# Optimization experiments

Measured on AMD Instinct MI355X. Metric: run time of the kernel, lower is better.

The kernel has to match this reference:

```python
import jax, jax.numpy as jnp
import numpy as np

N_COMPANY = 16384
N_SECTOR = 64
PER_SECTOR = N_COMPANY // N_SECTOR  # 256, companies grouped contiguously by sector
WIN = 32
D_IN = 16
H_GRU = 64
H_INTRA = 64
H_INTER = 64
D_OUT = 4
E_INNER = 524288  # avg degree 32 within sectors


def setup_inputs() -> dict:
    key = jax.random.key(0)
    ks = jax.random.split(key, 20)
    s = 0.05

    daily_data_batch = jax.random.normal(ks[0], (WIN, N_COMPANY, D_IN), jnp.float32)

    rng = np.random.default_rng(0)
    dst = rng.integers(0, N_COMPANY, E_INNER)
    src = (dst // PER_SECTOR) * PER_SECTOR + rng.integers(0, PER_SECTOR, E_INNER)  # same-sector neighbors
    inner_edge = jnp.asarray(np.stack([src, dst]), jnp.int32)

    a, b = np.meshgrid(np.arange(N_SECTOR), np.arange(N_SECTOR), indexing="ij")
    oe = np.stack([a.ravel(), b.ravel()])
    oe = oe[:, oe[0] != oe[1]]  # fully-connected sector graph w/o self loops (GAT adds them)
    outer_edge = jnp.asarray(oe, jnp.int32)

    sector_ids = jnp.asarray(np.arange(N_COMPANY) // PER_SECTOR, jnp.int32)

    inp = {
        "daily_data_batch": daily_data_batch,
        "inner_edge": inner_edge,
        "outer_edge": outer_edge,
        "sector_ids": sector_ids,
        # BatchNorm1d(input_dim*window_size)
        "bn_gamma": jnp.ones((D_IN * WIN,), jnp.float32),
        "bn_beta": jnp.zeros((D_IN * WIN,), jnp.float32),
        # Graph GRU (per-node learnable initial hidden state)
        "gru_Wih": s * jax.random.normal(ks[1], (D_IN, 3 * H_GRU), jnp.float32),
        "gru_Whh": s * jax.random.normal(ks[2], (H_GRU, 3 * H_GRU), jnp.float32),
        "gru_bih": jnp.zeros((3 * H_GRU,), jnp.float32),
        "gru_bhh": jnp.zeros((3 * H_GRU,), jnp.float32),
        "gru_h0": s * jax.random.normal(ks[3], (N_COMPANY, H_GRU), jnp.float32),
        # intra-sector GATConv
        "gat1_W": s * jax.random.normal(ks[4], (H_GRU, H_INTRA), jnp.float32),
        "gat1_asrc": s * jax.random.normal(ks[5], (H_INTRA,), jnp.float32),
        "gat1_adst": s * jax.random.normal(ks[6], (H_INTRA,), jnp.float32),
        "gat1_b": jnp.zeros((H_INTRA,), jnp.float32),
        # inter-sector GATConv
        "gat2_W": s * jax.random.normal(ks[7], (H_INTRA, H_INTER), jnp.float32),
        "gat2_asrc": s * jax.random.normal(ks[8], (H_INTER,), jnp.float32),
        "gat2_adst": s * jax.random.normal(ks[9], (H_INTER,), jnp.float32),
        "gat2_b": jnp.zeros((H_INTER,), jnp.float32),
        # fusion / logit heads
        "fusion_W": s * jax.random.normal(ks[10], (H_GRU + H_INTRA + H_INTER, H_GRU), jnp.float32),
        "fusion_b": jnp.zeros((H_GRU,), jnp.float32),
        "logit_W": s * jax.random.normal(ks[11], (H_GRU, D_OUT), jnp.float32),
        "logit_b": jnp.zeros((D_OUT,), jnp.float32),
    }
    return inp


def _gat(x, edge, W, a_src, a_dst, b):
    """PyG-style single-head GATConv with default add_self_loops=True."""
    N = x.shape[0]
    h = x @ W  # [N, F]
    loops = jnp.arange(N, dtype=edge.dtype)
    src = jnp.concatenate([edge[0], loops])
    dst = jnp.concatenate([edge[1], loops])
    e = jax.nn.leaky_relu(h[src] @ a_src + h[dst] @ a_dst, 0.2)  # [E]
    # segment softmax over incoming edges per dst node
    m = jax.ops.segment_max(e, dst, num_segments=N)
    ex = jnp.exp(e - m[dst])
    denom = jax.ops.segment_sum(ex, dst, num_segments=N)
    alpha = ex / (denom[dst] + 1e-16)
    out = jax.ops.segment_sum(h[src] * alpha[:, None], dst, num_segments=N)
    return out + b


def _forward(daily_data_batch, inner_edge, outer_edge, sector_ids,
             bn_gamma, bn_beta,
             gru_Wih, gru_Whh, gru_bih, gru_bhh, gru_h0,
             gat1_W, gat1_asrc, gat1_adst, gat1_b,
             gat2_W, gat2_asrc, gat2_adst, gat2_b,
             fusion_W, fusion_b, logit_W, logit_b):
    W, N, D = daily_data_batch.shape
    # BatchNorm1d over companies (train-mode batch stats, eps=1e-5)
    xb = jnp.transpose(daily_data_batch, (1, 0, 2)).reshape(N, W * D)
    mu = xb.mean(axis=0)
    var = xb.var(axis=0)
    xb = (xb - mu) * jax.lax.rsqrt(var + 1e-5) * bn_gamma + bn_beta
    x = jnp.transpose(xb.reshape(N, W, D), (1, 0, 2))  # [W, N, D]

    # GRU over the window, per-node hidden state
    def step(h, xt):
        gi = xt @ gru_Wih + gru_bih
        gh = h @ gru_Whh + gru_bhh
        ir, iz, inn = jnp.split(gi, 3, axis=-1)
        hr, hz, hn = jnp.split(gh, 3, axis=-1)
        r = jax.nn.sigmoid(ir + hr)
        z = jax.nn.sigmoid(iz + hz)
        n = jnp.tanh(inn + r * hn)
        return (1.0 - z) * n + z * h, None

    seq_emb, _ = jax.lax.scan(step, gru_h0, x)  # [N, H_GRU]

    intra_emb = _gat(seq_emb, inner_edge, gat1_W, gat1_asrc, gat1_adst, gat1_b)  # [N, H_INTRA]

    # sector_separater + per-sector max pooling == segment_max
    sec_pool = jax.ops.segment_max(intra_emb, sector_ids, num_segments=N_SECTOR)  # [S, H_INTRA]
    sec_emb = _gat(sec_pool, outer_edge, gat2_W, gat2_asrc, gat2_adst, gat2_b)  # [S, H_INTER]
    sec_broad = sec_emb[sector_ids]  # repeat_interleave back to companies

    fusion_vec = jnp.concatenate([seq_emb, sec_broad, intra_emb], axis=-1)
    fusion_vec = jax.nn.relu(fusion_vec @ fusion_W + fusion_b)
    logits = jax.nn.softmax(fusion_vec @ logit_W + logit_b, axis=1)
    logits = jnp.cumsum(logits, axis=1)
    eps = 5e-08
    return jnp.clip(logits, eps, 1.0 - eps)


def reference(daily_data_batch, inner_edge, outer_edge, sector_ids,
              bn_gamma, bn_beta,
              gru_Wih, gru_Whh, gru_bih, gru_bhh, gru_h0,
              gat1_W, gat1_asrc, gat1_adst, gat1_b,
              gat2_W, gat2_asrc, gat2_adst, gat2_b,
              fusion_W, fusion_b, logit_W, logit_b):
    return _forward(daily_data_batch, inner_edge, outer_edge, sector_ids,
                    bn_gamma, bn_beta,
                    gru_Wih, gru_Whh, gru_bih, gru_bhh, gru_h0,
                    gat1_W, gat1_asrc, gat1_adst, gat1_b,
                    gat2_W, gat2_asrc, gat2_adst, gat2_b,
                    fusion_W, fusion_b, logit_W, logit_b)
```

## Files before the change

### kernel.cpp

```cpp
#include <hip/hip_runtime.h>

#define NC 16384
#define WIN 32
#define DI 16
#define EI 524288

typedef unsigned short u16;
typedef unsigned char u8;
typedef unsigned int u32;
typedef __attribute__((ext_vector_type(8))) short bfrag8;
typedef __attribute__((ext_vector_type(4))) float facc4;

__device__ __forceinline__ float bf2f(u16 u) { return __uint_as_float(((u32)u) << 16); }
__device__ __forceinline__ u16 f2bf(float f) {
    u32 u = __float_as_uint(f);
    u += 0x7FFFu + ((u >> 16) & 1u);
    return (u16)(u >> 16);
}
__device__ __forceinline__ float frcp(float x) { return __builtin_amdgcn_rcpf(x); }
__device__ __forceinline__ float ex2(float x) {
#if __has_builtin(__builtin_amdgcn_exp2f)
    return __builtin_amdgcn_exp2f(x);
#else
    return __expf(x * 0.69314718055994531f);
#endif
}
__device__ __forceinline__ u32 pk2bf(float a, float b) {
    u32 r;
    asm("v_cvt_pk_bf16_f32 %0, %1, %2" : "=v"(r) : "v"(a), "v"(b));
    return r;
}
__device__ __forceinline__ float lrelu(float x) { return x >= 0.0f ? x : 0.2f * x; }
__device__ __forceinline__ float loadf(const void* p, size_t i, bool f32) {
    return f32 ? ((const float*)p)[i] : bf2f(((const u16*)p)[i]);
}
__device__ __forceinline__ bool is_f32(const void* gamma) {
    return ((const u32*)gamma)[0] == 0x3F800000u;
}
__device__ __forceinline__ int hswz(int f, int s) { return s ^ (((f >> 3) & 3) << 3); }

#define O_WIMG  1024
#define O_BIMG  10240
#define O_BIH   16384
#define O_BHH   16576
#define O_G1W   16768
#define O_G1AS  20864
#define O_G1AD  20928
#define O_G1B   20992
#define O_G2W   21056
#define O_G2AS  25152
#define O_G2AD  25216
#define O_G2B   25280
#define O_FB    25344
#define O_LW    25408
#define O_LB    25664
#define O_FW16  25668
#define O_BNACC 31812
#define O_SEQ   40960
#define O_H1    1089536
#define O_INTRA 1613824
#define O_SPOOL 2138112
#define O_AS    2170880
#define O_AD    2187264
#define O_M     2203648

__global__ __launch_bounds__(256) void k_convert(const void* __restrict__ daily,
                                                 const int* __restrict__ edges,
                                                 u32* __restrict__ M32,
                                                 const void* __restrict__ gamma,
                                                 const void* __restrict__ wih,
                                                 const void* __restrict__ whh,
                                                 const void* __restrict__ bih,
                                                 const void* __restrict__ bhh,
                                                 const void* __restrict__ g1w,
                                                 const void* __restrict__ g1as,
                                                 const void* __restrict__ g1ad,
                                                 const void* __restrict__ g1b,
                                                 const void* __restrict__ g2w,
                                                 const void* __restrict__ g2as,
                                                 const void* __restrict__ g2ad,
                                                 const void* __restrict__ g2b,
                                                 const void* __restrict__ fw,
                                                 const void* __restrict__ fb,
                                                 const void* __restrict__ lw,
                                                 const void* __restrict__ lb,
                                                 float* __restrict__ ws) {
    __shared__ float rS[256 * 17];
    __shared__ float rQ[256 * 17];
    __shared__ float sOut[2][16][16];
    int bid = blockIdx.x;
    int tid = threadIdx.x;
    int gt = bid * 256 + tid;
    const int GS = 640 * 256;
    bool f32 = is_f32(gamma);
    const float KR = -1.4426950408889634f;
    const float KN = -2.8853900817779268f;

    if (bid >= 128) {
        int g = (bid - 128) * 256 + tid;
        int4 s4 = ((const int4*)edges)[g];
        int4 d4 = ((const int4*)(edges + EI))[g];
        int ss[4] = {s4.x, s4.y, s4.z, s4.w};
        int dd[4] = {d4.x, d4.y, d4.z, d4.w};
#pragma unroll
        for (int i = 0; i < 4; i++) {
            int sl = ss[i] & 255;
            atomicAdd(&M32[dd[i] * 64 + (sl >> 2)], 1u << ((sl & 3) * 8));
        }
        return;
    }

    u16* fw16 = (u16*)(ws + O_FW16);
    for (int i = gt; i < 12288; i += GS)
        fw16[i] = f32 ? f2bf(((const float*)fw)[i]) : ((const u16*)fw)[i];
    for (int i = gt; i < 4096; i += GS) {
        ws[O_G1W + i] = loadf(g1w, i, f32);
        ws[O_G2W + i] = loadf(g2w, i, f32);
    }
    if (gt < 64) {
        ws[O_G1AS + gt] = loadf(g1as, gt, f32);
        ws[O_G1AD + gt] = loadf(g1ad, gt, f32);
        ws[O_G1B + gt] = loadf(g1b, gt, f32);
        ws[O_G2AS + gt] = loadf(g2as, gt, f32);
        ws[O_G2AD + gt] = loadf(g2ad, gt, f32);
        ws[O_G2B + gt] = loadf(g2b, gt, f32);
        ws[O_FB + gt] = loadf(fb, gt, f32);
    }
    if (gt < 256) ws[O_LW + gt] = loadf(lw, gt, f32);
    if (gt < 4) ws[O_LB + gt] = loadf(lb, gt, f32);

    for (int i = gt; i < 9216; i += GS) {
        int trow = i / 36;
        int idx = i % 36;
        int w_ = trow >> 6, lane_ = trow & 63, li_ = lane_ & 15, q_ = lane_ >> 4;
        u16 lo, hi;
        if (idx < 24) {
            int g = idx >> 3, kc = (idx >> 2) & 1, j2 = idx & 3;
            float sc = (g < 2) ? KR : KN;
            int col = g * 64 + w_ * 16 + li_;
            int k = kc * 32 + q_ * 8 + j2 * 2;
            lo = f2bf(sc * loadf(whh, (size_t)k * 192 + col, f32));
            hi = f2bf(sc * loadf(whh, (size_t)(k + 1) * 192 + col, f32));
        } else {
            int idx2 = idx - 24;
            int g = idx2 >> 2, j2 = idx2 & 3;
            float sc = (g < 2) ? KR : KN;
            int col = g * 64 + w_ * 16 + li_;
            int k = q_ * 8 + j2 * 2;
            lo = (k < 16) ? f2bf(sc * loadf(wih, (size_t)k * 192 + col, f32)) : (u16)0;
            hi = (k + 1 < 16) ? f2bf(sc * loadf(wih, (size_t)(k + 1) * 192 + col, f32)) : (u16)0;
        }
        ((u32*)(ws + O_WIMG))[i] = (u32)lo | ((u32)hi << 16);
    }
    for (int i = gt; i < 1024; i += GS) {
        int trow = i >> 2, e = i & 3;
        int w_ = trow >> 6, lane_ = trow & 63, li_ = lane_ & 15;
        int c = w_ * 16 + li_;
        float v;
        if (e == 0) v = KR * (loadf(bih, c, f32) + loadf(bhh, c, f32));
        else if (e == 1) v = KR * (loadf(bih, 64 + c, f32) + loadf(bhh, 64 + c, f32));
        else if (e == 2) v = KN * loadf(bih, 128 + c, f32);
        else v = KN * loadf(bhh, 128 + c, f32);
        ws[O_BIMG + i] = v;
    }

    {
        int w = bid >> 2, ch = bid & 3;
        float s[16], q[16];
#pragma unroll
        for (int i = 0; i < 16; i++) { s[i] = 0.f; q[i] = 0.f; }
        for (int it = 0; it < 16; it++) {
            int c = ch * 4096 + it * 256 + tid;
            size_t base = ((size_t)w * NC + c) * DI;
            float v[16];
            if (f32) {
                const float4* p = (const float4*)((const float*)daily + base);
                float4 a = p[0], b = p[1], cc = p[2], d = p[3];
                v[0] = a.x; v[1] = a.y; v[2] = a.z; v[3] = a.w;
                v[4] = b.x; v[5] = b.y; v[6] = b.z; v[7] = b.w;
                v[8] = cc.x; v[9] = cc.y; v[10] = cc.z; v[11] = cc.w;
                v[12] = d.x; v[13] = d.y; v[14] = d.z; v[15] = d.w;
            } else {
                const uint4* p = (const uint4*)((const u16*)daily + base);
                uint4 a = p[0], b = p[1];
                u32 us[8] = {a.x, a.y, a.z, a.w, b.x, b.y, b.z, b.w};
#pragma unroll
                for (int i = 0; i < 8; i++) {
                    v[2 * i] = __uint_as_float(us[i] << 16);
                    v[2 * i + 1] = __uint_as_float(us[i] & 0xFFFF0000u);
                }
            }
#pragma unroll
            for (int i = 0; i < 16; i++) { s[i] += v[i]; q[i] += v[i] * v[i]; }
        }
#pragma unroll
        for (int i = 0; i < 16; i++) { rS[tid * 17 + i] = s[i]; rQ[tid * 17 + i] = q[i]; }
        __syncthreads();
        int f = tid & 15, g = tid >> 4;
        float ss = 0.f, qq = 0.f;
        for (int t = g * 16; t < g * 16 + 16; t++) { ss += rS[t * 17 + f]; qq += rQ[t * 17 + f]; }
        sOut[0][g][f] = ss;
        sOut[1][g][f] = qq;
        __syncthreads();
        if (tid < 16) {
            float S = 0.f, Q = 0.f;
#pragma unroll
            for (int g2 = 0; g2 < 16; g2++) { S += sOut[0][g2][tid]; Q += sOut[1][g2][tid]; }
            ws[O_BNACC + ch * 512 + w * 16 + tid] = S;
            ws[O_BNACC + 2048 + ch * 512 + w * 16 + tid] = Q;
        }
    }
}

__global__ __launch_bounds__(256) void k_gru(const void* __restrict__ daily,
                                             const void* __restrict__ gamma,
                                             const void* __restrict__ beta,
                                             const void* __restrict__ h0_g,
                                             const float* __restrict__ ws,
                                             float* __restrict__ seq_out,
                                             u16* __restrict__ h1_out,
                                             float* __restrict__ asg,
                                             float* __restrict__ adg) {
    __shared__ __attribute__((aligned(16))) u16 sHd[2][16 * 72];
    __shared__ __attribute__((aligned(16))) u16 sXall[512 * 24];
    __shared__ float sSc[512], sSh[512];
    __shared__ float sRed[2][4][16];
    int tid = threadIdx.x;
    int w = tid >> 6, lane = tid & 63;
    int li = lane & 15, q = lane >> 4;
    int n0 = blockIdx.x * 16;
    int colw = w * 16 + li;
    bool f32 = is_f32(gamma);

    for (int f = tid; f < 512; f += 256) {
        float S = ws[O_BNACC + f] + ws[O_BNACC + 512 + f] + ws[O_BNACC + 1024 + f] + ws[O_BNACC + 1536 + f];
        float Q = ws[O_BNACC + 2048 + f] + ws[O_BNACC + 2560 + f] + ws[O_BNACC + 3072 + f] + ws[O_BNACC + 3584 + f];
        float mu = S * (1.0f / NC);
        float var = Q * (1.0f / NC) - mu * mu;
        float sc = loadf(gamma, f, f32) * rsqrtf(var + 1e-5f);
        sSc[f] = sc;
        sSh[f] = loadf(beta, f, f32) - mu * sc;
    }
    __syncthreads();

    for (int R = tid; R < 512; R += 256) {
        int t = R >> 4, m = R & 15;
        size_t base = ((size_t)t * NC + n0 + m) * DI;
        float xv[16];
        if (f32) {
            const float4* p = (const float4*)((const float*)daily + base);
            float4 a = p[0], b = p[1], c = p[2], d = p[3];
            xv[0] = a.x; xv[1] = a.y; xv[2] = a.z; xv[3] = a.w;
            xv[4] = b.x; xv[5] = b.y; xv[6] = b.z; xv[7] = b.w;
            xv[8] = c.x; xv[9] = c.y; xv[10] = c.z; xv[11] = c.w;
            xv[12] = d.x; xv[13] = d.y; xv[14] = d.z; xv[15] = d.w;
        } else {
            const uint4* p = (const uint4*)((const u16*)daily + base);
            uint4 a = p[0], b = p[1];
            u32 us[8] = {a.x, a.y, a.z, a.w, b.x, b.y, b.z, b.w};
#pragma unroll
            for (int i = 0; i < 8; i++) {
                xv[2 * i] = __uint_as_float(us[i] << 16);
                xv[2 * i + 1] = __uint_as_float(us[i] & 0xFFFF0000u);
            }
        }
        u32 pxu[8];
#pragma unroll
        for (int i = 0; i < 16; i += 2)
            pxu[i >> 1] = pk2bf(xv[i] * sSc[t * 16 + i] + sSh[t * 16 + i],
                                xv[i + 1] * sSc[t * 16 + i + 1] + sSh[t * 16 + i + 1]);
        *(uint4*)&sXall[R * 24] = *(const uint4*)&pxu[0];
        *(uint4*)&sXall[R * 24 + 8] = *(const uint4*)&pxu[4];
    }

    bfrag8 bh[3][2];
    bfrag8 bx[3];
    {
        const bfrag8* wf = (const bfrag8*)((const char*)(ws + O_WIMG) + (size_t)tid * 144);
        int c_ = 0;
#pragma unroll
        for (int g = 0; g < 3; g++)
#pragma unroll
            for (int kc = 0; kc < 2; kc++) bh[g][kc] = wf[c_++];
#pragma unroll
        for (int g = 0; g < 3; g++) bx[g] = wf[c_++];
    }
    float bR, bZ, bNX, bNH;
    {
        float4 b0 = ((const float4*)(ws + O_BIMG))[tid];
        bR = b0.x; bZ = b0.y; bNX = b0.z; bNH = b0.w;
    }

    float hC[4];
#pragma unroll
    for (int r = 0; r < 4; r++)
        hC[r] = loadf(h0_g, (size_t)(n0 + q * 4 + r) * 64 + colw, f32);
    {
        int hr = tid >> 4, hc = (tid & 15) * 4;
        u32 a = pk2bf(loadf(h0_g, (size_t)(n0 + hr) * 64 + hc, f32),
                      loadf(h0_g, (size_t)(n0 + hr) * 64 + hc + 1, f32));
        u32 b = pk2bf(loadf(h0_g, (size_t)(n0 + hr) * 64 + hc + 2, f32),
                      loadf(h0_g, (size_t)(n0 + hr) * 64 + hc + 3, f32));
        uint2 v2; v2.x = a; v2.y = b;
        *(uint2*)&sHd[0][hr * 72 + hc] = v2;
    }
    __syncthreads();

    bfrag8 ax = (bfrag8){0, 0, 0, 0, 0, 0, 0, 0};
    if (q < 2) ax = *(const bfrag8*)&sXall[li * 24 + q * 8];
    for (int t = 0; t < WIN; t++) {
        int p = t & 1;
        bfrag8 ah0 = *(const bfrag8*)&sHd[p][li * 72 + q * 8];
        bfrag8 ah1 = *(const bfrag8*)&sHd[p][li * 72 + 32 + q * 8];
        int tn = (t + 1) & (WIN - 1);
        bfrag8 axn = (bfrag8){0, 0, 0, 0, 0, 0, 0, 0};
        if (q < 2) axn = *(const bfrag8*)&sXall[(tn * 16 + li) * 24 + q * 8];
        facc4 aR = __builtin_amdgcn_mfma_f32_16x16x32_bf16(ax, bx[0], (facc4){bR, bR, bR, bR}, 0, 0, 0);
        facc4 aZ = __builtin_amdgcn_mfma_f32_16x16x32_bf16(ax, bx[1], (facc4){bZ, bZ, bZ, bZ}, 0, 0, 0);
        facc4 aNX = __builtin_amdgcn_mfma_f32_16x16x32_bf16(ax, bx[2], (facc4){bNX, bNX, bNX, bNX}, 0, 0, 0);
        facc4 aNH = __builtin_amdgcn_mfma_f32_16x16x32_bf16(ah0, bh[2][0], (facc4){bNH, bNH, bNH, bNH}, 0, 0, 0);
        aR = __builtin_amdgcn_mfma_f32_16x16x32_bf16(ah0, bh[0][0], aR, 0, 0, 0);
        aZ = __builtin_amdgcn_mfma_f32_16x16x32_bf16(ah0, bh[1][0], aZ, 0, 0, 0);
        aNH = __builtin_amdgcn_mfma_f32_16x16x32_bf16(ah1, bh[2][1], aNH, 0, 0, 0);
        aR = __builtin_amdgcn_mfma_f32_16x16x32_bf16(ah1, bh[0][1], aR, 0, 0, 0);
        aZ = __builtin_amdgcn_mfma_f32_16x16x32_bf16(ah1, bh[1][1], aZ, 0, 0, 0);
#pragma unroll
        for (int r = 0; r < 4; r++) {
            float gr = frcp(1.0f + ex2(aR[r]));
            float gz = frcp(1.0f + ex2(aZ[r]));
            float narg = aNX[r] + gr * aNH[r];
            float gn = 2.0f * frcp(1.0f + ex2(narg)) - 1.0f;
            hC[r] = gn + gz * (hC[r] - gn);
        }
#pragma unroll
        for (int rp = 0; rp < 4; rp += 2) {
            u32 pk = pk2bf(hC[rp], hC[rp + 1]);
            sHd[p ^ 1][(q * 4 + rp) * 72 + colw] = (u16)pk;
            sHd[p ^ 1][(q * 4 + rp + 1) * 72 + colw] = (u16)(pk >> 16);
        }
        __syncthreads();
        ax = axn;
    }

#pragma unroll
    for (int r = 0; r < 4; r++)
        seq_out[(size_t)(n0 + q * 4 + r) * 64 + colw] = hC[r];

    bfrag8 a0 = *(const bfrag8*)&sHd[0][li * 72 + q * 8];
    bfrag8 a1 = *(const bfrag8*)&sHd[0][li * 72 + 32 + q * 8];
    const facc4 zf = {0.f, 0.f, 0.f, 0.f};
    bfrag8 bg0, bg1;
#pragma unroll
    for (int j = 0; j < 8; j++) {
        bg0[j] = (short)f2bf(ws[O_G1W + (q * 8 + j) * 64 + colw]);
        bg1[j] = (short)f2bf(ws[O_G1W + (32 + q * 8 + j) * 64 + colw]);
    }
    facc4 acc = __builtin_amdgcn_mfma_f32_16x16x32_bf16(a0, bg0, zf, 0, 0, 0);
    acc = __builtin_amdgcn_mfma_f32_16x16x32_bf16(a1, bg1, acc, 0, 0, 0);
    float a1s_j = ws[O_G1AS + colw], a1d_j = ws[O_G1AD + colw];
    float pAs[4], pAd[4];
#pragma unroll
    for (int r = 0; r < 4; r++) {
        h1_out[(size_t)(n0 + q * 4 + r) * 64 + colw] = f2bf(acc[r]);
        pAs[r] = acc[r] * a1s_j;
        pAd[r] = acc[r] * a1d_j;
    }
#pragma unroll
    for (int o = 1; o < 16; o <<= 1)
#pragma unroll
        for (int r = 0; r < 4; r++) {
            pAs[r] += __shfl_xor(pAs[r], o);
            pAd[r] += __shfl_xor(pAd[r], o);
        }
    if (li == 0) {
#pragma unroll
        for (int r = 0; r < 4; r++) {
            sRed[0][w][q * 4 + r] = pAs[r];
            sRed[1][w][q * 4 + r] = pAd[r];
        }
    }
    __syncthreads();
    if (tid < 16) {
        asg[n0 + tid] = sRed[0][0][tid] + sRed[0][1][tid] + sRed[0][2][tid] + sRed[0][3][tid];
        adg[n0 + tid] = sRed[1][0][tid] + sRed[1][1][tid] + sRed[1][2][tid] + sRed[1][3][tid];
    }
}

__global__ __launch_bounds__(256) void k_gat1agg(const u16* __restrict__ h1g,
                                                 const float* __restrict__ ws,
                                                 const u8* __restrict__ M8,
                                                 const float* __restrict__ asg,
                                                 const float* __restrict__ adg,
                                                 u16* __restrict__ intra,
                                                 float* __restrict__ spool8) {
    __shared__ __attribute__((aligned(16))) u16 hT[64 * 264];
    __shared__ __attribute__((aligned(16))) u16 sP[32 * 264];
    __shared__ float sAs[256], sAd[32], sB[64], sRS[32];
    __shared__ float sRSp[8][32];
    __shared__ float wmax[4];
    int tid = threadIdx.x;
    int sector = blockIdx.x >> 3;
    int dstbase = sector * 256 + (blockIdx.x & 7) * 32;
    int sbase = sector * 256;
    {
#pragma unroll
        for (int p = 0; p < 8; p++) {
            int row = p * 32 + (tid >> 3);
            int c0 = (tid & 7) * 8;
            uint4 v = *(const uint4*)(h1g + (size_t)(sbase + row) * 64 + c0);
            u16 e[8];
            *(uint4*)e = v;
#pragma unroll
            for (int i = 0; i < 8; i++) {
                int f = c0 + i;
                hT[f * 264 + hswz(f, row)] = e[i];
            }
        }
    }
    sAs[tid] = asg[sbase + tid];
    if (tid < 32) sAd[tid] = adg[dstbase + tid];
    if (tid < 64) sB[tid] = ws[O_G1B + tid];
    __syncthreads();
    int lane = tid & 63, w = tid >> 6;
    int li = lane & 15, q = lane >> 4;
    {
        float a = sAs[tid];
#pragma unroll
        for (int o = 1; o < 64; o <<= 1) a = fmaxf(a, __shfl_xor(a, o));
        if (lane == 0) wmax[w] = a;
    }
    __syncthreads();
    float maxA = fmaxf(fmaxf(wmax[0], wmax[1]), fmaxf(wmax[2], wmax[3]));

    int prow = tid >> 3, pcg = tid & 7;
    {
        float adr_p = sAd[prow];
        float mrow_p = lrelu(maxA + adr_p);
        float lsum = 0.f;
        const u8* mp = M8 + (size_t)(dstbase + prow) * 256 + pcg * 32;
        uint4 mva = *(const uint4*)mp;
        uint4 mvb = *(const uint4*)(mp + 16);
        u32 wsrc[8] = {mva.x, mva.y, mva.z, mva.w, mvb.x, mvb.y, mvb.z, mvb.w};
#pragma unroll
        for (int i2 = 0; i2 < 16; i2++) {
            int i0 = 2 * i2;
            u32 mb0 = (wsrc[i0 >> 2] >> ((i0 & 3) * 8)) & 255u;
            u32 mb1 = (wsrc[i0 >> 2] >> (((i0 + 1) & 3) * 8)) & 255u;
            int c = pcg * 32 + i0;
            float e0 = lrelu(sAs[c] + adr_p);
            float e1 = lrelu(sAs[c + 1] + adr_p);
            float v0 = (float)mb0 * __expf(e0 - mrow_p);
            float v1 = (float)mb1 * __expf(e1 - mrow_p);
            u16 b0 = f2bf(v0), b1 = f2bf(v1);
            *(u32*)&sP[prow * 264 + pcg * 32 + i0] = (u32)b0 | ((u32)b1 << 16);
            lsum += bf2f(b0) + bf2f(b1);
        }
        sRSp[pcg][prow] = lsum;
    }
    __syncthreads();

    facc4 acc[2];
    acc[0] = (facc4){0.f, 0.f, 0.f, 0.f};
    acc[1] = (facc4){0.f, 0.f, 0.f, 0.f};
#pragma unroll
    for (int kc = 0; kc < 8; kc++) {
        int fB = w * 16 + li;
        bfrag8 bfh = *(const bfrag8*)&hT[fB * 264 + hswz(fB, kc * 32 + q * 8)];
#pragma unroll
        for (int mt = 0; mt < 2; mt++) {
            bfrag8 af = *(const bfrag8*)&sP[(mt * 16 + li) * 264 + kc * 32 + q * 8];
            acc[mt] = __builtin_amdgcn_mfma_f32_16x16x32_bf16(af, bfh, acc[mt], 0, 0, 0);
        }
    }
    if (tid < 32) {
        float s = 0.f;
#pragma unroll
        for (int g = 0; g < 8; g++) s += sRSp[g][tid];
        sRS[tid] = s;
    }
    __syncthreads();

    float vmax = -1e30f;
    int colL = w * 16 + li;
#pragma unroll
    for (int mt = 0; mt < 2; mt++) {
#pragma unroll
        for (int r = 0; r < 4; r++) {
            int row = mt * 16 + q * 4 + r;
            int d = dstbase + row;
            int selfI = (blockIdx.x & 7) * 32 + row;
            float adr = sAd[row];
            float es = lrelu(sAs[selfI] + adr);
            float mrow = lrelu(maxA + adr);
            float exS = __expf(es - mrow);
            float denom = sRS[row] + exS;
            float inv = frcp(denom + 1e-16f);
            float selfh = bf2f(hT[colL * 264 + hswz(colL, selfI)]);
            float val = (acc[mt][r] + exS * selfh) * inv + sB[colL];
            intra[(size_t)d * 64 + colL] = f2bf(val);
            vmax = fmaxf(vmax, val);
        }
    }
    vmax = fmaxf(vmax, __shfl_xor(vmax, 16));
    vmax = fmaxf(vmax, __shfl_xor(vmax, 32));
    if (q == 0) spool8[(size_t)blockIdx.x * 64 + colL] = vmax;
}

__global__ __launch_bounds__(256) void k_fusion(const float* __restrict__ seq,
                                                const float* __restrict__ spool8,
                                                const u16* __restrict__ intra,
                                                const float* __restrict__ ws,
                                                const void* __restrict__ gamma,
                                                void* __restrict__ out) {
    __shared__ __attribute__((aligned(16))) union {
        struct { u16 sPmax[64 * 72]; float sH2[64 * 68]; } p0;
        struct { u16 sV[64 * 200]; float sFus[64 * 68]; } p1;
    } U;
    __shared__ float sSemb[64], sAs2[64], sAd2[64];
    __shared__ float sFB[64], sLW[256], sLB[4];
    __shared__ float red2[512];
    int tid = threadIdx.x, n0 = blockIdx.x * 64;
    int sid = blockIdx.x >> 2;
    bool f32 = is_f32(gamma);
    int lane = tid & 63, w = tid >> 6;
    int li = lane & 15, q = lane >> 4;
    int colw = w * 16 + li;

    for (int i = tid; i < 4096; i += 256) {
        int n = i >> 6, k = i & 63;
        const float* pp = &spool8[(size_t)(n * 8) * 64 + k];
        float m = pp[0];
#pragma unroll
        for (int p = 1; p < 8; p++) m = fmaxf(m, pp[p * 64]);
        U.p0.sPmax[n * 72 + k] = f2bf(m);
    }
    bfrag8 bw2[2];
#pragma unroll
    for (int kc = 0; kc < 2; kc++)
#pragma unroll
        for (int j = 0; j < 8; j++)
            bw2[kc][j] = (short)f2bf(ws[O_G2W + (kc * 32 + q * 8 + j) * 64 + colw]);
    __syncthreads();
    {
        const facc4 zf = {0.f, 0.f, 0.f, 0.f};
#pragma unroll
        for (int mt = 0; mt < 4; mt++) {
            bfrag8 af0 = *(const bfrag8*)&U.p0.sPmax[(mt * 16 + li) * 72 + q * 8];
            bfrag8 af1 = *(const bfrag8*)&U.p0.sPmax[(mt * 16 + li) * 72 + 32 + q * 8];
            facc4 a2 = __builtin_amdgcn_mfma_f32_16x16x32_bf16(af0, bw2[0], zf, 0, 0, 0);
            a2 = __builtin_amdgcn_mfma_f32_16x16x32_bf16(af1, bw2[1], a2, 0, 0, 0);
#pragma unroll
            for (int r = 0; r < 4; r++)
                U.p0.sH2[(mt * 16 + q * 4 + r) * 68 + colw] = a2[r];
        }
    }
    __syncthreads();
    {
        int n = tid >> 2, jg = tid & 3, j0 = jg * 16;
        float ps = 0.f, pd = 0.f;
#pragma unroll
        for (int i = 0; i < 16; i++) {
            float v = U.p0.sH2[n * 68 + j0 + i];
            ps += v * ws[O_G2AS + j0 + i];
            pd += v * ws[O_G2AD + j0 + i];
        }
        red2[(n * 4 + jg) * 2] = ps;
        red2[(n * 4 + jg) * 2 + 1] = pd;
    }
    __syncthreads();
    if (tid < 64) {
        float s = 0.f, dd = 0.f;
        for (int g = 0; g < 4; g++) { s += red2[(tid * 4 + g) * 2]; dd += red2[(tid * 4 + g) * 2 + 1]; }
        sAs2[tid] = s; sAd2[tid] = dd;
    }
    __syncthreads();
    if (tid < 64) {
        float e = lrelu(sAs2[tid] + sAd2[sid]);
        float m = e;
        for (int o = 32; o; o >>= 1) m = fmaxf(m, __shfl_xor(m, o));
        float ex = __expf(e - m);
        float den = ex;
        for (int o = 32; o; o >>= 1) den += __shfl_xor(den, o);
        float inv = frcp(den + 1e-16f);
        float o_ = 0.f;
        for (int l = 0; l < 64; l++) {
            float a = __shfl(ex, l);
            o_ += a * U.p0.sH2[l * 68 + tid];
        }
        sSemb[tid] = o_ * inv + ws[O_G2B + tid];
    }
    if (tid < 64) sFB[tid] = ws[O_FB + tid];
    sLW[tid] = ws[O_LW + tid];
    if (tid < 4) sLB[tid] = ws[O_LB + tid];
    __syncthreads();

    {
        int c = tid >> 2, p = tid & 3;
        u16 px[16];
        const float* rp = seq + (size_t)(n0 + c) * 64 + p * 16;
#pragma unroll
        for (int i = 0; i < 16; i += 4) {
            float4 v = *(const float4*)&rp[i];
            px[i] = f2bf(v.x); px[i + 1] = f2bf(v.y); px[i + 2] = f2bf(v.z); px[i + 3] = f2bf(v.w);
        }
        *(uint4*)&U.p1.sV[c * 200 + p * 16] = *(const uint4*)&px[0];
        *(uint4*)&U.p1.sV[c * 200 + p * 16 + 8] = *(const uint4*)&px[8];
#pragma unroll
        for (int i = 0; i < 16; i++) px[i] = f2bf(sSemb[p * 16 + i]);
        *(uint4*)&U.p1.sV[c * 200 + 64 + p * 16] = *(const uint4*)&px[0];
        *(uint4*)&U.p1.sV[c * 200 + 64 + p * 16 + 8] = *(const uint4*)&px[8];
        const u16* ip = intra + (size_t)(n0 + c) * 64 + p * 16;
        *(uint4*)&U.p1.sV[c * 200 + 128 + p * 16] = *(const uint4*)ip;
        *(uint4*)&U.p1.sV[c * 200 + 128 + p * 16 + 8] = *(const uint4*)(ip + 8);
    }
    const u16* fw16g = (const u16*)(ws + O_FW16);
    bfrag8 bwf[6];
#pragma unroll
    for (int kc = 0; kc < 6; kc++)
#pragma unroll
        for (int j = 0; j < 8; j++)
            bwf[kc][j] = (short)fw16g[(kc * 32 + q * 8 + j) * 64 + colw];
    __syncthreads();

    facc4 acc[4];
#pragma unroll
    for (int mt = 0; mt < 4; mt++) acc[mt] = (facc4){0.f, 0.f, 0.f, 0.f};
#pragma unroll
    for (int kc = 0; kc < 6; kc++) {
#pragma unroll
        for (int mt = 0; mt < 4; mt++) {
            bfrag8 av = *(const bfrag8*)&U.p1.sV[(mt * 16 + li) * 200 + kc * 32 + q * 8];
            acc[mt] = __builtin_amdgcn_mfma_f32_16x16x32_bf16(av, bwf[kc], acc[mt], 0, 0, 0);
        }
    }
    float fb = sFB[colw];
#pragma unroll
    for (int mt = 0; mt < 4; mt++)
#pragma unroll
        for (int r = 0; r < 4; r++) {
            float v = fmaxf(acc[mt][r] + fb, 0.f);
            U.p1.sFus[(mt * 16 + q * 4 + r) * 68 + colw] = v;
        }
    __syncthreads();

    {
        int cpy = tid >> 2, cls = tid & 3;
        float lv = sLB[cls];
        for (int j = 0; j < 64; j++) lv += U.p1.sFus[cpy * 68 + j] * sLW[j * 4 + cls];
        float m2 = fmaxf(lv, __shfl_xor(lv, 1));
        m2 = fmaxf(m2, __shfl_xor(m2, 2));
        float e = __expf(lv - m2);
        float s2 = e + __shfl_xor(e, 1);
        s2 += __shfl_xor(s2, 2);
        float is = frcp(s2);
        float pref = e;
        float t1 = __shfl_up(pref, 1);
        if (cls >= 1) pref += t1;
        float t2 = __shfl_up(pref, 2);
        if (cls >= 2) pref += t2;
        float ck = pref * is;
        const float lo = 5e-8f, hi = 1.0f - 5e-8f;
        ck = fminf(fmaxf(ck, lo), hi);
        size_t ob = (size_t)(n0 + cpy) * 4 + cls;
        if (f32) ((float*)out)[ob] = ck;
        else ((u16*)out)[ob] = f2bf(ck);
    }
}

extern "C" void kernel_launch(void* const* d_in, const int* in_sizes, int n_in,
                              void* d_out, int out_size, void* d_ws, size_t ws_size,
                              hipStream_t stream) {
    const void* daily = d_in[0];
    const int* inner = (const int*)d_in[1];
    const void* gamma = d_in[4];
    const void* beta = d_in[5];
    const void* wih = d_in[6];
    const void* whh = d_in[7];
    const void* bih = d_in[8];
    const void* bhh = d_in[9];
    const void* h0 = d_in[10];
    const void* g1w = d_in[11];
    const void* g1as = d_in[12];
    const void* g1ad = d_in[13];
    const void* g1b = d_in[14];
    const void* g2w = d_in[15];
    const void* g2as = d_in[16];
    const void* g2ad = d_in[17];
    const void* g2b = d_in[18];
    const void* fw = d_in[19];
    const void* fb = d_in[20];
    const void* lw = d_in[21];
    const void* lb = d_in[22];

    float* ws = (float*)d_ws;
    u16* h1g = (u16*)(ws + O_H1);
    u16* intra = (u16*)(ws + O_INTRA);
    u8* M8 = (u8*)(ws + O_M);

    hipMemsetAsync(M8, 0, (size_t)NC * 256, stream);
    k_convert<<<640, 256, 0, stream>>>(daily, inner, (u32*)M8, gamma, wih, whh, bih, bhh,
                                       g1w, g1as, g1ad, g1b, g2w, g2as, g2ad, g2b,
                                       fw, fb, lw, lb, ws);
    k_gru<<<1024, 256, 0, stream>>>(daily, gamma, beta, h0, ws, ws + O_SEQ, h1g, ws + O_AS, ws + O_AD);
    k_gat1agg<<<512, 256, 0, stream>>>(h1g, ws, M8, ws + O_AS, ws + O_AD, intra, ws + O_SPOOL);
    k_fusion<<<256, 256, 0, stream>>>(ws + O_SEQ, ws + O_SPOOL, intra, ws, gamma, d_out);
}
```

Before: 208.1 us.

## Merge GAT aggregation and fusion into one cooperative kernel with grid sync

```diff
diff --git a/kernel.cpp b/kernel.cpp
--- a/kernel.cpp
+++ b/kernel.cpp
@@ -1,4 +1,7 @@
 #include <hip/hip_runtime.h>
+#include <hip/hip_cooperative_groups.h>
+
+namespace cg = cooperative_groups;
 
 #define NC 16384
 #define WIN 32
@@ -386,284 +389,294 @@
     }
 }
 
-__global__ __launch_bounds__(256) void k_gat1agg(const u16* __restrict__ h1g,
-                                                 const float* __restrict__ ws,
-                                                 const u8* __restrict__ M8,
-                                                 const float* __restrict__ asg,
-                                                 const float* __restrict__ adg,
-                                                 u16* __restrict__ intra,
-                                                 float* __restrict__ spool8) {
-    __shared__ __attribute__((aligned(16))) u16 hT[64 * 264];
-    __shared__ __attribute__((aligned(16))) u16 sP[32 * 264];
-    __shared__ float sAs[256], sAd[32], sB[64], sRS[32];
-    __shared__ float sRSp[8][32];
-    __shared__ float wmax[4];
+__global__ void k_gatfus(const u16* __restrict__ h1g,
+                         const float* __restrict__ ws,
+                         const u8* __restrict__ M8,
+                         const float* __restrict__ asg,
+                         const float* __restrict__ adg,
+                         u16* __restrict__ intra,
+                         float* __restrict__ spool8,
+                         const float* __restrict__ seq,
+                         const void* __restrict__ gamma,
+                         void* __restrict__ out) {
+    __shared__ __attribute__((aligned(16))) union {
+        struct {
+            u16 hT[64 * 264];
+            u16 sP[32 * 264];
+            float sAs[256], sAd[32], sB[64], sRS[32];
+            float sRSp[8][32];
+            float wmax[4];
+        } a;
+        struct {
+            union {
+                struct { u16 sPmax[64 * 72]; float sH2[64 * 68]; } p0;
+                struct { u16 sV[64 * 200]; float sFus[64 * 68]; } p1;
+            } U;
+            float sSemb[64], sAs2[64], sAd2[64];
+            float sFB[64], sLW[256], sLB[4];
+            float red2[512];
+        } b;
+    } L;
+    cg::grid_group grid = cg::this_grid();
     int tid = threadIdx.x;
-    int sector = blockIdx.x >> 3;
-    int dstbase = sector * 256 + (blockIdx.x & 7) * 32;
-    int sbase = sector * 256;
-    {
-#pragma unroll
-        for (int p = 0; p < 8; p++) {
-            int row = p * 32 + (tid >> 3);
-            int c0 = (tid & 7) * 8;
-            uint4 v = *(const uint4*)(h1g + (size_t)(sbase + row) * 64 + c0);
-            u16 e[8];
-            *(uint4*)e = v;
-#pragma unroll
-            for (int i = 0; i < 8; i++) {
-                int f = c0 + i;
-                hT[f * 264 + hswz(f, row)] = e[i];
-            }
-        }
-    }
-    sAs[tid] = asg[sbase + tid];
-    if (tid < 32) sAd[tid] = adg[dstbase + tid];
-    if (tid < 64) sB[tid] = ws[O_G1B + tid];
-    __syncthreads();
-    int lane = tid & 63, w = tid >> 6;
-    int li = lane & 15, q = lane >> 4;
-    {
-        float a = sAs[tid];
-#pragma unroll
-        for (int o = 1; o < 64; o <<= 1) a = fmaxf(a, __shfl_xor(a, o));
-        if (lane == 0) wmax[w] = a;
-    }
-    __syncthreads();
-    float maxA = fmaxf(fmaxf(wmax[0], wmax[1]), fmaxf(wmax[2], wmax[3]));
-
-    int prow = tid >> 3, pcg = tid & 7;
-    {
-        float adr_p = sAd[prow];
-        float mrow_p = lrelu(maxA + adr_p);
-        float lsum = 0.f;
-        const u8* mp = M8 + (size_t)(dstbase + prow) * 256 + pcg * 32;
-        uint4 mva = *(const uint4*)mp;
-        uint4 mvb = *(const uint4*)(mp + 16);
-        u32 wsrc[8] = {mva.x, mva.y, mva.z, mva.w, mvb.x, mvb.y, mvb.z, mvb.w};
-#pragma unroll
-        for (int i2 = 0; i2 < 16; i2++) {
-            int i0 = 2 * i2;
-            u32 mb0 = (wsrc[i0 >> 2] >> ((i0 & 3) * 8)) & 255u;
-            u32 mb1 = (wsrc[i0 >> 2] >> (((i0 + 1) & 3) * 8)) & 255u;
-            int c = pcg * 32 + i0;
-            float e0 = lrelu(sAs[c] + adr_p);
-            float e1 = lrelu(sAs[c + 1] + adr_p);
-            float v0 = (float)mb0 * __expf(e0 - mrow_p);
-            float v1 = (float)mb1 * __expf(e1 - mrow_p);
-            u16 b0 = f2bf(v0), b1 = f2bf(v1);
-            *(u32*)&sP[prow * 264 + pcg * 32 + i0] = (u32)b0 | ((u32)b1 << 16);
-            lsum += bf2f(b0) + bf2f(b1);
-        }
-        sRSp[pcg][prow] = lsum;
-    }
-    __syncthreads();
-
-    facc4 acc[2];
-    acc[0] = (facc4){0.f, 0.f, 0.f, 0.f};
-    acc[1] = (facc4){0.f, 0.f, 0.f, 0.f};
-#pragma unroll
-    for (int kc = 0; kc < 8; kc++) {
-        int fB = w * 16 + li;
-        bfrag8 bfh = *(const bfrag8*)&hT[fB * 264 + hswz(fB, kc * 32 + q * 8)];
-#pragma unroll
-        for (int mt = 0; mt < 2; mt++) {
-            bfrag8 af = *(const bfrag8*)&sP[(mt * 16 + li) * 264 + kc * 32 + q * 8];
-            acc[mt] = __builtin_amdgcn_mfma_f32_16x16x32_bf16(af, bfh, acc[mt], 0, 0, 0);
-        }
-    }
-    if (tid < 32) {
-        float s = 0.f;
-#pragma unroll
-        for (int g = 0; g < 8; g++) s += sRSp[g][tid];
-        sRS[tid] = s;
-    }
-    __syncthreads();
-
-    float vmax = -1e30f;
-    int colL = w * 16 + li;
-#pragma unroll
-    for (int mt = 0; mt < 2; mt++) {
-#pragma unroll
-        for (int r = 0; r < 4; r++) {
-            int row = mt * 16 + q * 4 + r;
-            int d = dstbase + row;
-            int selfI = (blockIdx.x & 7) * 32 + row;
-            float adr = sAd[row];
-            float es = lrelu(sAs[selfI] + adr);
-            float mrow = lrelu(maxA + adr);
-            float exS = __expf(es - mrow);
-            float denom = sRS[row] + exS;
-            float inv = frcp(denom + 1e-16f);
-            float selfh = bf2f(hT[colL * 264 + hswz(colL, selfI)]);
-            float val = (acc[mt][r] + exS * selfh) * inv + sB[colL];
-            intra[(size_t)d * 64 + colL] = f2bf(val);
-            vmax = fmaxf(vmax, val);
-        }
-    }
-    vmax = fmaxf(vmax, __shfl_xor(vmax, 16));
-    vmax = fmaxf(vmax, __shfl_xor(vmax, 32));
-    if (q == 0) spool8[(size_t)blockIdx.x * 64 + colL] = vmax;
-}
-
-__global__ __launch_bounds__(256) void k_fusion(const float* __restrict__ seq,
-                                                const float* __restrict__ spool8,
-                                                const u16* __restrict__ intra,
-                                                const float* __restrict__ ws,
-                                                const void* __restrict__ gamma,
-                                                void* __restrict__ out) {
-    __shared__ __attribute__((aligned(16))) union {
-        struct { u16 sPmax[64 * 72]; float sH2[64 * 68]; } p0;
-        struct { u16 sV[64 * 200]; float sFus[64 * 68]; } p1;
-    } U;
-    __shared__ float sSemb[64], sAs2[64], sAd2[64];
-    __shared__ float sFB[64], sLW[256], sLB[4];
-    __shared__ float red2[512];
-    int tid = threadIdx.x, n0 = blockIdx.x * 64;
-    int sid = blockIdx.x >> 2;
     bool f32 = is_f32(gamma);
     int lane = tid & 63, w = tid >> 6;
     int li = lane & 15, q = lane >> 4;
-    int colw = w * 16 + li;
-
-    for (int i = tid; i < 4096; i += 256) {
-        int n = i >> 6, k = i & 63;
-        const float* pp = &spool8[(size_t)(n * 8) * 64 + k];
-        float m = pp[0];
-#pragma unroll
-        for (int p = 1; p < 8; p++) m = fmaxf(m, pp[p * 64]);
-        U.p0.sPmax[n * 72 + k] = f2bf(m);
-    }
-    bfrag8 bw2[2];
-#pragma unroll
-    for (int kc = 0; kc < 2; kc++)
-#pragma unroll
-        for (int j = 0; j < 8; j++)
-            bw2[kc][j] = (short)f2bf(ws[O_G2W + (kc * 32 + q * 8 + j) * 64 + colw]);
-    __syncthreads();
+
     {
-        const facc4 zf = {0.f, 0.f, 0.f, 0.f};
-#pragma unroll
-        for (int mt = 0; mt < 4; mt++) {
-            bfrag8 af0 = *(const bfrag8*)&U.p0.sPmax[(mt * 16 + li) * 72 + q * 8];
-            bfrag8 af1 = *(const bfrag8*)&U.p0.sPmax[(mt * 16 + li) * 72 + 32 + q * 8];
-            facc4 a2 = __builtin_amdgcn_mfma_f32_16x16x32_bf16(af0, bw2[0], zf, 0, 0, 0);
-            a2 = __builtin_amdgcn_mfma_f32_16x16x32_bf16(af1, bw2[1], a2, 0, 0, 0);
-#pragma unroll
-            for (int r = 0; r < 4; r++)
-                U.p0.sH2[(mt * 16 + q * 4 + r) * 68 + colw] = a2[r];
-        }
-    }
-    __syncthreads();
+        int sector = blockIdx.x >> 3;
+        int dstbase = sector * 256 + (blockIdx.x & 7) * 32;
+        int sbase = sector * 256;
+        {
+#pragma unroll
+            for (int p = 0; p < 8; p++) {
+                int row = p * 32 + (tid >> 3);
+                int c0 = (tid & 7) * 8;
+                uint4 v = *(const uint4*)(h1g + (size_t)(sbase + row) * 64 + c0);
+                u16 e[8];
+                *(uint4*)e = v;
+#pragma unroll
+                for (int i = 0; i < 8; i++) {
+                    int f = c0 + i;
+                    L.a.hT[f * 264 + hswz(f, row)] = e[i];
+                }
+            }
+        }
+        L.a.sAs[tid] = asg[sbase + tid];
+        if (tid < 32) L.a.sAd[tid] = adg[dstbase + tid];
+        if (tid < 64) L.a.sB[tid] = ws[O_G1B + tid];
+        __syncthreads();
+        {
+            float a = L.a.sAs[tid];
+#pragma unroll
+            for (int o = 1; o < 64; o <<= 1) a = fmaxf(a, __shfl_xor(a, o));
+            if (lane == 0) L.a.wmax[w] = a;
+        }
+        __syncthreads();
+        float maxA = fmaxf(fmaxf(L.a.wmax[0], L.a.wmax[1]), fmaxf(L.a.wmax[2], L.a.wmax[3]));
+
+        int prow = tid >> 3, pcg = tid & 7;
+        {
+            float adr_p = L.a.sAd[prow];
+            float mrow_p = lrelu(maxA + adr_p);
+            float lsum = 0.f;
+            const u8* mp = M8 + (size_t)(dstbase + prow) * 256 + pcg * 32;
+            uint4 mva = *(const uint4*)mp;
+            uint4 mvb = *(const uint4*)(mp + 16);
+            u32 wsrc[8] = {mva.x, mva.y, mva.z, mva.w, mvb.x, mvb.y, mvb.z, mvb.w};
+#pragma unroll
+            for (int i2 = 0; i2 < 16; i2++) {
+                int i0 = 2 * i2;
+                u32 mb0 = (wsrc[i0 >> 2] >> ((i0 & 3) * 8)) & 255u;
+                u32 mb1 = (wsrc[i0 >> 2] >> (((i0 + 1) & 3) * 8)) & 255u;
+                int c = pcg * 32 + i0;
+                float e0 = lrelu(L.a.sAs[c] + adr_p);
+                float e1 = lrelu(L.a.sAs[c + 1] + adr_p);
+                float v0 = (float)mb0 * __expf(e0 - mrow_p);
+                float v1 = (float)mb1 * __expf(e1 - mrow_p);
+                u16 b0 = f2bf(v0), b1 = f2bf(v1);
+                *(u32*)&L.a.sP[prow * 264 + pcg * 32 + i0] = (u32)b0 | ((u32)b1 << 16);
+                lsum += bf2f(b0) + bf2f(b1);
+            }
+            L.a.sRSp[pcg][prow] = lsum;
+        }
+        __syncthreads();
+
+        facc4 acc[2];
+        acc[0] = (facc4){0.f, 0.f, 0.f, 0.f};
+        acc[1] = (facc4){0.f, 0.f, 0.f, 0.f};
+#pragma unroll
+        for (int kc = 0; kc < 8; kc++) {
+            int fB = w * 16 + li;
+            bfrag8 bfh = *(const bfrag8*)&L.a.hT[fB * 264 + hswz(fB, kc * 32 + q * 8)];
+#pragma unroll
+            for (int mt = 0; mt < 2; mt++) {
+                bfrag8 af = *(const bfrag8*)&L.a.sP[(mt * 16 + li) * 264 + kc * 32 + q * 8];
+                acc[mt] = __builtin_amdgcn_mfma_f32_16x16x32_bf16(af, bfh, acc[mt], 0, 0, 0);
+            }
+        }
+        if (tid < 32) {
+            float s = 0.f;
+#pragma unroll
+            for (int g = 0; g < 8; g++) s += L.a.sRSp[g][tid];
+            L.a.sRS[tid] = s;
+        }
+        __syncthreads();
+
+        float vmax = -1e30f;
+        int colL = w * 16 + li;
+#pragma unroll
+        for (int mt = 0; mt < 2; mt++) {
+#pragma unroll
+            for (int r = 0; r < 4; r++) {
+                int row = mt * 16 + q * 4 + r;
+                int d = dstbase + row;
+                int selfI = (blockIdx.x & 7) * 32 + row;
+                float adr = L.a.sAd[row];
+                float es = lrelu(L.a.sAs[selfI] + adr);
+                float mrow = lrelu(maxA + adr);
+                float exS = __expf(es - mrow);
+                float denom = L.a.sRS[row] + exS;
+                float inv = frcp(denom + 1e-16f);
+                float selfh = bf2f(L.a.hT[colL * 264 + hswz(colL, selfI)]);
+                float val = (acc[mt][r] + exS * selfh) * inv + L.a.sB[colL];
+                intra[(size_t)d * 64 + colL] = f2bf(val);
+                vmax = fmaxf(vmax, val);
+            }
+        }
+        vmax = fmaxf(vmax, __shfl_xor(vmax, 16));
+        vmax = fmaxf(vmax, __shfl_xor(vmax, 32));
+        if (q == 0) spool8[(size_t)blockIdx.x * 64 + colL] = vmax;
+    }
+
+    __threadfence();
+    grid.sync();
+    if (blockIdx.x >= 256) return;
+
     {
-        int n = tid >> 2, jg = tid & 3, j0 = jg * 16;
-        float ps = 0.f, pd = 0.f;
-#pragma unroll
-        for (int i = 0; i < 16; i++) {
-            float v = U.p0.sH2[n * 68 + j0 + i];
-            ps += v * ws[O_G2AS + j0 + i];
-            pd += v * ws[O_G2AD + j0 + i];
-        }
-        red2[(n * 4 + jg) * 2] = ps;
-        red2[(n * 4 + jg) * 2 + 1] = pd;
-    }
-    __syncthreads();
-    if (tid < 64) {
-        float s = 0.f, dd = 0.f;
-        for (int g = 0; g < 4; g++) { s += red2[(tid * 4 + g) * 2]; dd += red2[(tid * 4 + g) * 2 + 1]; }
-        sAs2[tid] = s; sAd2[tid] = dd;
-    }
-    __syncthreads();
-    if (tid < 64) {
-        float e = lrelu(sAs2[tid] + sAd2[sid]);
-        float m = e;
-        for (int o = 32; o; o >>= 1) m = fmaxf(m, __shfl_xor(m, o));
-        float ex = __expf(e - m);
-        float den = ex;
-        for (int o = 32; o; o >>= 1) den += __shfl_xor(den, o);
-        float inv = frcp(den + 1e-16f);
-        float o_ = 0.f;
-        for (int l = 0; l < 64; l++) {
-            float a = __shfl(ex, l);
-            o_ += a * U.p0.sH2[l * 68 + tid];
-        }
-        sSemb[tid] = o_ * inv + ws[O_G2B + tid];
-    }
-    if (tid < 64) sFB[tid] = ws[O_FB + tid];
-    sLW[tid] = ws[O_LW + tid];
-    if (tid < 4) sLB[tid] = ws[O_LB + tid];
-    __syncthreads();
-
-    {
-        int c = tid >> 2, p = tid & 3;
-        u16 px[16];
-        const float* rp = seq + (size_t)(n0 + c) * 64 + p * 16;
-#pragma unroll
-        for (int i = 0; i < 16; i += 4) {
-            float4 v = *(const float4*)&rp[i];
-            px[i] = f2bf(v.x); px[i + 1] = f2bf(v.y); px[i + 2] = f2bf(v.z); px[i + 3] = f2bf(v.w);
-        }
-        *(uint4*)&U.p1.sV[c * 200 + p * 16] = *(const uint4*)&px[0];
-        *(uint4*)&U.p1.sV[c * 200 + p * 16 + 8] = *(const uint4*)&px[8];
-#pragma unroll
-        for (int i = 0; i < 16; i++) px[i] = f2bf(sSemb[p * 16 + i]);
-        *(uint4*)&U.p1.sV[c * 200 + 64 + p * 16] = *(const uint4*)&px[0];
-        *(uint4*)&U.p1.sV[c * 200 + 64 + p * 16 + 8] = *(const uint4*)&px[8];
-        const u16* ip = intra + (size_t)(n0 + c) * 64 + p * 16;
-        *(uint4*)&U.p1.sV[c * 200 + 128 + p * 16] = *(const uint4*)ip;
-        *(uint4*)&U.p1.sV[c * 200 + 128 + p * 16 + 8] = *(const uint4*)(ip + 8);
-    }
-    const u16* fw16g = (const u16*)(ws + O_FW16);
-    bfrag8 bwf[6];
-#pragma unroll
-    for (int kc = 0; kc < 6; kc++)
-#pragma unroll
-        for (int j = 0; j < 8; j++)
-            bwf[kc][j] = (short)fw16g[(kc * 32 + q * 8 + j) * 64 + colw];
-    __syncthreads();
-
-    facc4 acc[4];
-#pragma unroll
-    for (int mt = 0; mt < 4; mt++) acc[mt] = (facc4){0.f, 0.f, 0.f, 0.f};
-#pragma unroll
-    for (int kc = 0; kc < 6; kc++) {
-#pragma unroll
-        for (int mt = 0; mt < 4; mt++) {
-            bfrag8 av = *(const bfrag8*)&U.p1.sV[(mt * 16 + li) * 200 + kc * 32 + q * 8];
-            acc[mt] = __builtin_amdgcn_mfma_f32_16x16x32_bf16(av, bwf[kc], acc[mt], 0, 0, 0);
-        }
-    }
-    float fb = sFB[colw];
-#pragma unroll
-    for (int mt = 0; mt < 4; mt++)
-#pragma unroll
-        for (int r = 0; r < 4; r++) {
-            float v = fmaxf(acc[mt][r] + fb, 0.f);
-            U.p1.sFus[(mt * 16 + q * 4 + r) * 68 + colw] = v;
-        }
-    __syncthreads();
-
-    {
-        int cpy = tid >> 2, cls = tid & 3;
-        float lv = sLB[cls];
-        for (int j = 0; j < 64; j++) lv += U.p1.sFus[cpy * 68 + j] * sLW[j * 4 + cls];
-        float m2 = fmaxf(lv, __shfl_xor(lv, 1));
-        m2 = fmaxf(m2, __shfl_xor(m2, 2));
-        float e = __expf(lv - m2);
-        float s2 = e + __shfl_xor(e, 1);
-        s2 += __shfl_xor(s2, 2);
-        float is = frcp(s2);
-        float pref = e;
-        float t1 = __shfl_up(pref, 1);
-        if (cls >= 1) pref += t1;
-        float t2 = __shfl_up(pref, 2);
-        if (cls >= 2) pref += t2;
-        float ck = pref * is;
-        const float lo = 5e-8f, hi = 1.0f - 5e-8f;
-        ck = fminf(fmaxf(ck, lo), hi);
-        size_t ob = (size_t)(n0 + cpy) * 4 + cls;
-        if (f32) ((float*)out)[ob] = ck;
-        else ((u16*)out)[ob] = f2bf(ck);
+        int n0 = blockIdx.x * 64;
+        int sid = blockIdx.x >> 2;
+        int colw = w * 16 + li;
+
+        for (int i = tid; i < 4096; i += 256) {
+            int n = i >> 6, k = i & 63;
+            const float* pp = &spool8[(size_t)(n * 8) * 64 + k];
+            float m = pp[0];
+#pragma unroll
+            for (int p = 1; p < 8; p++) m = fmaxf(m, pp[p * 64]);
+            L.b.U.p0.sPmax[n * 72 + k] = f2bf(m);
+        }
+        bfrag8 bw2[2];
+#pragma unroll
+        for (int kc = 0; kc < 2; kc++)
+#pragma unroll
+            for (int j = 0; j < 8; j++)
+                bw2[kc][j] = (short)f2bf(ws[O_G2W + (kc * 32 + q * 8 + j) * 64 + colw]);
+        __syncthreads();
+        {
+            const facc4 zf = {0.f, 0.f, 0.f, 0.f};
+#pragma unroll
+            for (int mt = 0; mt < 4; mt++) {
+                bfrag8 af0 = *(const bfrag8*)&L.b.U.p0.sPmax[(mt * 16 + li) * 72 + q * 8];
+                bfrag8 af1 = *(const bfrag8*)&L.b.U.p0.sPmax[(mt * 16 + li) * 72 + 32 + q * 8];
+                facc4 a2 = __builtin_amdgcn_mfma_f32_16x16x32_bf16(af0, bw2[0], zf, 0, 0, 0);
+                a2 = __builtin_amdgcn_mfma_f32_16x16x32_bf16(af1, bw2[1], a2, 0, 0, 0);
+#pragma unroll
+                for (int r = 0; r < 4; r++)
+                    L.b.U.p0.sH2[(mt * 16 + q * 4 + r) * 68 + colw] = a2[r];
+            }
+        }
+        __syncthreads();
+        {
+            int n = tid >> 2, jg = tid & 3, j0 = jg * 16;
+            float ps = 0.f, pd = 0.f;
+#pragma unroll
+            for (int i = 0; i < 16; i++) {
+                float v = L.b.U.p0.sH2[n * 68 + j0 + i];
+                ps += v * ws[O_G2AS + j0 + i];
+                pd += v * ws[O_G2AD + j0 + i];
+            }
+            L.b.red2[(n * 4 + jg) * 2] = ps;
+            L.b.red2[(n * 4 + jg) * 2 + 1] = pd;
+        }
+        __syncthreads();
+        if (tid < 64) {
+            float s = 0.f, dd = 0.f;
+            for (int g = 0; g < 4; g++) { s += L.b.red2[(tid * 4 + g) * 2]; dd += L.b.red2[(tid * 4 + g) * 2 + 1]; }
+            L.b.sAs2[tid] = s; L.b.sAd2[tid] = dd;
+        }
+        __syncthreads();
+        if (tid < 64) {
+            float e = lrelu(L.b.sAs2[tid] + L.b.sAd2[sid]);
+            float m = e;
+            for (int o = 32; o; o >>= 1) m = fmaxf(m, __shfl_xor(m, o));
+            float ex = __expf(e - m);
+            float den = ex;
+            for (int o = 32; o; o >>= 1) den += __shfl_xor(den, o);
+            float inv = frcp(den + 1e-16f);
+            float o_ = 0.f;
+            for (int l = 0; l < 64; l++) {
+                float a = __shfl(ex, l);
+                o_ += a * L.b.U.p0.sH2[l * 68 + tid];
+            }
+            L.b.sSemb[tid] = o_ * inv + ws[O_G2B + tid];
+        }
+        if (tid < 64) L.b.sFB[tid] = ws[O_FB + tid];
+        L.b.sLW[tid] = ws[O_LW + tid];
+        if (tid < 4) L.b.sLB[tid] = ws[O_LB + tid];
+        __syncthreads();
+
+        {
+            int c = tid >> 2, p = tid & 3;
+            u16 px[16];
+            const float* rp = seq + (size_t)(n0 + c) * 64 + p * 16;
+#pragma unroll
+            for (int i = 0; i < 16; i += 4) {
+                float4 v = *(const float4*)&rp[i];
+                px[i] = f2bf(v.x); px[i + 1] = f2bf(v.y); px[i + 2] = f2bf(v.z); px[i + 3] = f2bf(v.w);
+            }
+            *(uint4*)&L.b.U.p1.sV[c * 200 + p * 16] = *(const uint4*)&px[0];
+            *(uint4*)&L.b.U.p1.sV[c * 200 + p * 16 + 8] = *(const uint4*)&px[8];
+#pragma unroll
+            for (int i = 0; i < 16; i++) px[i] = f2bf(L.b.sSemb[p * 16 + i]);
+            *(uint4*)&L.b.U.p1.sV[c * 200 + 64 + p * 16] = *(const uint4*)&px[0];
+            *(uint4*)&L.b.U.p1.sV[c * 200 + 64 + p * 16 + 8] = *(const uint4*)&px[8];
+            const u16* ip = intra + (size_t)(n0 + c) * 64 + p * 16;
+            *(uint4*)&L.b.U.p1.sV[c * 200 + 128 + p * 16] = *(const uint4*)ip;
+            *(uint4*)&L.b.U.p1.sV[c * 200 + 128 + p * 16 + 8] = *(const uint4*)(ip + 8);
+        }
+        const u16* fw16g = (const u16*)(ws + O_FW16);
+        bfrag8 bwf[6];
+#pragma unroll
+        for (int kc = 0; kc < 6; kc++)
+#pragma unroll
+            for (int j = 0; j < 8; j++)
+                bwf[kc][j] = (short)fw16g[(kc * 32 + q * 8 + j) * 64 + colw];
+        __syncthreads();
+
+        facc4 acc[4];
+#pragma unroll
+        for (int mt = 0; mt < 4; mt++) acc[mt] = (facc4){0.f, 0.f, 0.f, 0.f};
+#pragma unroll
+        for (int kc = 0; kc < 6; kc++) {
+#pragma unroll
+            for (int mt = 0; mt < 4; mt++) {
+                bfrag8 av = *(const bfrag8*)&L.b.U.p1.sV[(mt * 16 + li) * 200 + kc * 32 + q * 8];
+                acc[mt] = __builtin_amdgcn_mfma_f32_16x16x32_bf16(av, bwf[kc], acc[mt], 0, 0, 0);
+            }
+        }
+        float fb = L.b.sFB[colw];
+#pragma unroll
+        for (int mt = 0; mt < 4; mt++)
+#pragma unroll
+            for (int r = 0; r < 4; r++) {
+                float v = fmaxf(acc[mt][r] + fb, 0.f);
+                L.b.U.p1.sFus[(mt * 16 + q * 4 + r) * 68 + colw] = v;
+            }
+        __syncthreads();
+
+        {
+            int cpy = tid >> 2, cls = tid & 3;
+            float lv = L.b.sLB[cls];
+            for (int j = 0; j < 64; j++) lv += L.b.U.p1.sFus[cpy * 68 + j] * L.b.sLW[j * 4 + cls];
+            float m2 = fmaxf(lv, __shfl_xor(lv, 1));
+            m2 = fmaxf(m2, __shfl_xor(m2, 2));
+            float e = __expf(lv - m2);
+            float s2 = e + __shfl_xor(e, 1);
+            s2 += __shfl_xor(s2, 2);
+            float is = frcp(s2);
+            float pref = e;
+            float t1 = __shfl_up(pref, 1);
+            if (cls >= 1) pref += t1;
+            float t2 = __shfl_up(pref, 2);
+            if (cls >= 2) pref += t2;
+            float ck = pref * is;
+            const float lo = 5e-8f, hi = 1.0f - 5e-8f;
+            ck = fminf(fmaxf(ck, lo), hi);
+            size_t ob = (size_t)(n0 + cpy) * 4 + cls;
+            if (f32) ((float*)out)[ob] = ck;
+            else ((u16*)out)[ob] = f2bf(ck);
+        }
     }
 }
 
@@ -702,6 +715,19 @@
                                        g1w, g1as, g1ad, g1b, g2w, g2as, g2ad, g2b,
                                        fw, fb, lw, lb, ws);
     k_gru<<<1024, 256, 0, stream>>>(daily, gamma, beta, h0, ws, ws + O_SEQ, h1g, ws + O_AS, ws + O_AD);
-    k_gat1agg<<<512, 256, 0, stream>>>(h1g, ws, M8, ws + O_AS, ws + O_AD, intra, ws + O_SPOOL);
-    k_fusion<<<256, 256, 0, stream>>>(ws + O_SEQ, ws + O_SPOOL, intra, ws, gamma, d_out);
-}
+    {
+        const u16* h1c = h1g;
+        const float* wsc = ws;
+        const u8* m8c = M8;
+        const float* asgp = ws + O_AS;
+        const float* adgp = ws + O_AD;
+        u16* intrap = intra;
+        float* spoolp = ws + O_SPOOL;
+        const float* seqp = ws + O_SEQ;
+        const void* gammap = gamma;
+        void* outp = d_out;
+        void* kargs[] = {(void*)&h1c, (void*)&wsc, (void*)&m8c, (void*)&asgp, (void*)&adgp,
+                         (void*)&intrap, (void*)&spoolp, (void*)&seqp, (void*)&gammap, (void*)&outp};
+        hipLaunchCooperativeKernel((const void*)k_gatfus, dim3(512), dim3(256), kargs, 0, stream);
+    }
+}
```

Result: slower. 354.9 us (+70.6%).
